# Optimization experiments

Hardware: AMD Instinct MI355X
Metric: run time of the kernel (lower is better)

## Reference

```python
import jax, jax.numpy as jnp
import numpy as np

VARIANCES = jnp.array([0.1, 0.1, 0.2, 0.2], jnp.float32)
TOTAL_LABELS = 81
MAX_TOTAL = 200        # max_total_size (also max_output_size_per_class)
SCORE_T = 0.5          # score_threshold
IOU_T = 0.5            # tf combined_non_max_suppression default iou_threshold


def setup_inputs() -> dict:
    key = jax.random.key(0)
    k1, k2, k3, k4 = jax.random.split(key, 4)
    B, N, C = 8, 1000, TOTAL_LABELS
    # valid normalized RoIs: y1,x1 in [0,0.7), h,w in [0.01,0.31)
    yx1 = jax.random.uniform(k1, (B, N, 2), jnp.float32) * 0.7
    hw = jax.random.uniform(k2, (B, N, 2), jnp.float32) * 0.3 + 0.01
    roi_bboxes = jnp.concatenate([yx1, yx1 + hw], axis=-1)  # [y1,x1,y2,x2]
    pred_deltas = jax.random.normal(k3, (B, N, C * 4), jnp.float32) * 0.5
    pred_label_probs = jax.random.uniform(k4, (B, N, C), jnp.float32)
    return {"roi_bboxes": roi_bboxes, "pred_deltas": pred_deltas,
            "pred_label_probs": pred_label_probs}


def _decode(rois, deltas):
    # rois: [..., 4] (y1,x1,y2,x2); deltas: [..., 4] (dy,dx,dh,dw)
    h = rois[..., 2] - rois[..., 0]
    w = rois[..., 3] - rois[..., 1]
    cy = rois[..., 0] + 0.5 * h
    cx = rois[..., 1] + 0.5 * w
    ncy = deltas[..., 0] * h + cy
    ncx = deltas[..., 1] * w + cx
    nh = jnp.exp(deltas[..., 2]) * h
    nw = jnp.exp(deltas[..., 3]) * w
    return jnp.stack([ncy - 0.5 * nh, ncx - 0.5 * nw,
                      ncy + 0.5 * nh, ncx + 0.5 * nw], axis=-1)


def _nms_lane(boxes, scores):
    # greedy per-class NMS over one (batch, class) lane. boxes [N,4], scores [N]
    N = boxes.shape[0]
    order = jnp.argsort(-scores)
    b = boxes[order]
    s = scores[order]
    area = (b[:, 2] - b[:, 0]) * (b[:, 3] - b[:, 1])
    idx = jnp.arange(N)

    def body(i, keep):
        bi = b[i]
        iy1 = jnp.maximum(bi[0], b[:, 0])
        ix1 = jnp.maximum(bi[1], b[:, 1])
        iy2 = jnp.minimum(bi[2], b[:, 2])
        ix2 = jnp.minimum(bi[3], b[:, 3])
        inter = jnp.maximum(iy2 - iy1, 0.0) * jnp.maximum(ix2 - ix1, 0.0)
        iou = inter / (area[i] + area - inter + 1e-8)
        suppress = keep[i] & (iou > IOU_T) & (idx > i)
        return keep & ~suppress

    keep0 = s > SCORE_T                       # score filtering before NMS
    keep = jax.lax.fori_loop(0, N, body, keep0)
    keep = keep & (jnp.cumsum(keep) <= MAX_TOTAL)  # max_output_size_per_class
    return b, jnp.where(keep, s, 0.0)          # boxes in score order, masked scores


def _forward(roi_bboxes, pred_deltas, pred_label_probs):
    B, N, _ = pred_deltas.shape
    C = TOTAL_LABELS
    deltas = pred_deltas.reshape(B, N, C, 4) * VARIANCES
    boxes = _decode(roi_bboxes[:, :, None, :], deltas)          # [B,N,C,4]
    bg = jnp.argmax(pred_label_probs, axis=-1)[..., None] == 0  # background rows
    scores = jnp.where(bg, 0.0, pred_label_probs)               # [B,N,C]

    boxes_t = boxes.transpose(0, 2, 1, 3)   # [B,C,N,4]
    scores_t = scores.transpose(0, 2, 1)    # [B,C,N]
    b_s, s_s = jax.vmap(jax.vmap(_nms_lane))(boxes_t, scores_t)

    flat_s = s_s.reshape(B, C * N)
    flat_b = b_s.reshape(B, C * N, 4)
    cls = jnp.broadcast_to(jnp.arange(C)[:, None], (C, N)).reshape(C * N)

    top_s, top_i = jax.lax.top_k(flat_s, MAX_TOTAL)             # combined top-k
    top_b = jnp.take_along_axis(flat_b, top_i[..., None], axis=1)
    top_c = cls[top_i]

    valid = top_s > 0.0
    final_b = jnp.clip(jnp.where(valid[..., None], top_b, 0.0), 0.0, 1.0)
    final_c = jnp.where(valid, top_c, 0).astype(jnp.float32)
    final_s = jnp.where(valid, top_s, 0.0)
    return final_b, final_c, final_s


def reference(roi_bboxes, pred_deltas, pred_label_probs):
    return _forward(roi_bboxes, pred_deltas, pred_label_probs)
```

## Files before the change

### kernel.cpp

```cpp
#include <hip/hip_runtime.h>

#define NROI 1000
#define NCLS 81
#define NB   8
#define NLANE (NB*NCLS)
#define MAXM 1024
#define MAXKEEP 200
#define SCORE_T 0.5f
#define NT 512
#define NW 8
#define SCAP 1024
#define TROWS 125

typedef unsigned long long u64;
typedef unsigned int u32;


__device__ __forceinline__ void decode_box(const float* __restrict__ roi,
                                           const float* __restrict__ dl,
                                           float& oy1, float& ox1,
                                           float& oy2, float& ox2) {
#pragma clang fp contract(off)
  float y1 = roi[0], x1 = roi[1], y2 = roi[2], x2 = roi[3];
  float h = y2 - y1;
  float w = x2 - x1;
  float cy = y1 + 0.5f * h;
  float cx = x1 + 0.5f * w;
  float d0 = dl[0] * 0.1f;
  float d1 = dl[1] * 0.1f;
  float d2 = dl[2] * 0.2f;
  float d3 = dl[3] * 0.2f;
  float ncy = d0 * h + cy;
  float ncx = d1 * w + cx;
  float nh = expf(d2) * h;
  float nw = expf(d3) * w;
  oy1 = ncy - 0.5f * nh;
  ox1 = ncx - 0.5f * nw;
  oy2 = ncy + 0.5f * nh;
  ox2 = ncx + 0.5f * nw;
}

__device__ __forceinline__ float area_f(float4 bx) {
#pragma clang fp contract(off)
  return (bx.z - bx.x) * (bx.w - bx.y);
}

__device__ __forceinline__ bool hit_f(float4 bi, float ia, float4 bj, float ja) {
#pragma clang fp contract(off)
  float yy1 = fmaxf(bi.x, bj.x);
  float xx1 = fmaxf(bi.y, bj.y);
  float yy2 = fminf(bi.z, bj.z);
  float xx2 = fminf(bi.w, bj.w);
  float ih = fmaxf(yy2 - yy1, 0.0f);
  float iw = fmaxf(xx2 - xx1, 0.0f);
  float inter = ih * iw;
  float den = ia + ja;
  den = den - inter;
  den = den + 1e-8f;
  return (inter + inter) > den;
}

__device__ __forceinline__ u64 pack_key(u32 sbits, int flat, int n) {
  return ((u64)sbits << 32) | ((u64)(131071 - flat) << 15) | ((u64)n << 5);
}

__global__ __launch_bounds__(512) void prep_kernel(const float* __restrict__ probs,
                                                   float* __restrict__ probs_t,
                                                   int* __restrict__ bhist) {
  __shared__ float tile[TROWS * NCLS];
  __shared__ u32 bgf[TROWS];
  int blk = blockIdx.x;
  int tid = threadIdx.x;
  if (blk == 0) {
    for (int i = tid; i < NB * 256; i += 512) bhist[i] = 0;
  }
  int row0 = blk * TROWS;
  for (int i = tid; i < TROWS * NCLS; i += 512)
    tile[i] = probs[(size_t)row0 * NCLS + i];
  __syncthreads();
  if (tid < TROWS) {
    const float* r = &tile[tid * NCLS];
    float p0 = r[0], m = -1e30f;
    for (int c2 = 1; c2 < NCLS; ++c2) m = fmaxf(m, r[c2]);
    bgf[tid] = (p0 >= m) ? 1u : 0u;
  }
  __syncthreads();
  int b = row0 / NROI;
  int nbase = row0 - b * NROI;
  for (int j = tid; j < TROWS * NCLS; j += 512) {
    int c2 = j / TROWS, r = j - c2 * TROWS;
    float v = bgf[r] ? 0.0f : tile[r * NCLS + c2];
    probs_t[((size_t)(b * NCLS + c2)) * NROI + nbase + r] = v;
  }
}

__global__ __launch_bounds__(NT) void gather_nms_kernel(
    const float* __restrict__ roi, const float* __restrict__ deltas,
    const float* __restrict__ probs_t,
    int* __restrict__ keep_count, u64* __restrict__ lane_key,
    int* __restrict__ bhist) {
  int lane = (blockIdx.x % 8) * NCLS + blockIdx.x / 8;
  int b = lane / NCLS, c = lane % NCLS;
  int tid = threadIdx.x;
  int w = tid >> 6, l = tid & 63;

  __shared__ alignas(16) char smem[26624];
  float4* sbox   = (float4*)smem;
  u64*    skeyU  = (u64*)smem;
  u64*    skeyB  = (u64*)(smem + 8192);
  u64*    skey   = (u64*)(smem + 16384);
  int*    bcnt   = (int*)(smem + 24576);
  int*    bstart = (int*)(smem + 25600);
  __shared__ u64 hmask8[NW][64];
  __shared__ u64 suppm8[NW];
  __shared__ u64 keepmask[16];
  __shared__ int scount, segbase[16];

  if (tid == 0) scount = 0;
  if (tid < 256) bcnt[tid] = 0;
  __syncthreads();

  const float* pc = probs_t + ((size_t)(b * NCLS + c)) * NROI;
  for (int base_n = 0; base_n < NROI; base_n += NT) {
    int n = base_n + tid;
    float s = (n < NROI) ? pc[n] : 0.0f;
    bool cand = s > SCORE_T;
    u64 bal = __ballot(cand);
    int wb = 0;
    if (l == 0) wb = atomicAdd(&scount, (int)__popcll(bal));
    wb = __shfl(wb, 0);
    if (cand) {
      int off = (int)__popcll(bal & ((1ull << l) - 1ull));
      u32 sb = __float_as_uint(s);
      skeyU[wb + off] = ((u64)sb << 32) | (u64)(0xFFFFFFFFu - (u32)n);
      atomicAdd(&bcnt[(sb >> 15) & 255], 1);
    }
  }
  __syncthreads();
  int M = scount;
  int nchunks = (M + 63) >> 6;

  if (w == 0) {
    int d0 = 4 * l, d1 = d0 + 1, d2 = d0 + 2, d3 = d0 + 3;
    int c0 = bcnt[255 - d0], c1 = bcnt[255 - d1];
    int c2 = bcnt[255 - d2], c3 = bcnt[255 - d3];
    int t = c0 + c1 + c2 + c3;
    int inc = t;
    for (int off = 1; off < 64; off <<= 1) {
      int v = __shfl_up(inc, off);
      if (l >= off) inc += v;
    }
    int excl = inc - t;
    int s0 = excl, s1 = excl + c0, s2 = excl + c0 + c1, s3 = excl + c0 + c1 + c2;
    bcnt[255 - d0] = s0; bstart[255 - d0] = s0;
    bcnt[255 - d1] = s1; bstart[255 - d1] = s1;
    bcnt[255 - d2] = s2; bstart[255 - d2] = s2;
    bcnt[255 - d3] = s3; bstart[255 - d3] = s3;
  }
  __syncthreads();

  for (int p = tid; p < M; p += NT) {
    u64 k = skeyU[p];
    int bkt = (int)((k >> 47) & 255);
    int pos = atomicAdd(&bcnt[bkt], 1);
    skeyB[pos] = k;
  }
  __syncthreads();

  for (int p = tid; p < M; p += NT) {
    u64 k = skeyB[p];
    int bkt = (int)((k >> 47) & 255);
    int st = bstart[bkt], en = bcnt[bkt];
    int r = st;
    for (int q = st; q < en; ++q) r += (skeyB[q] > k) ? 1 : 0;
    skey[r] = k;
  }
  if (tid < 16) {
    int rem = M - (tid << 6);
    keepmask[tid] = (rem >= 64) ? ~0ull : ((rem <= 0) ? 0ull : ((1ull << rem) - 1ull));
  }
  __syncthreads();

  if (w == 7 && nchunks > 0) {
    u64 k = skey[l];
    int nn = (int)(0xFFFFFFFFu - (u32)(k & 0xFFFFFFFFull));
    int row = b * NROI + ((l < M) ? nn : 0);
    float by1, bx1, by2, bx2;
    decode_box(roi + (size_t)row * 4, deltas + ((size_t)row * NCLS + c) * 4,
               by1, bx1, by2, bx2);
    sbox[l] = make_float4(by1, bx1, by2, bx2);
  }
  __syncthreads();

  int kc = 0;
  const u64 stridemask = 0x0101010101010101ull << w;
  const u64 low = (1ull << l) - 1ull;
  for (int ck = 0; ck < nchunks; ++ck) {
    int start = ck << 6;
    float4 bj = sbox[start + l];
    float ja = area_f(bj);

    {
      u64 part = 0;
#pragma unroll
      for (int r = 0; r < 8; ++r) {
        int i = (w << 3) + r;
        float4 bi = sbox[start + i];
        float ia = area_f(bi);
        if (hit_f(bi, ia, bj, ja)) part |= (1ull << i);
      }
      hmask8[w][l] = part;
    }

    {
      bool supp = false;
      for (int q = 0; q < ck; ++q) {
        u64 mq = keepmask[q] & stridemask;
        while (mq) {
          int i = __ffsll((unsigned long long)mq) - 1;
          mq &= mq - 1;
          float4 bi = sbox[(q << 6) + i];
          float ia = area_f(bi);
          supp |= hit_f(bi, ia, bj, ja);
        }
      }
      u64 sb = __ballot(supp);
      if (l == 0) suppm8[w] = sb;
    }

    if (w == 7 && ck + 1 < nchunks) {
      int p = ((ck + 1) << 6) + l;
      u64 k = skey[p];
      int nn = (int)(0xFFFFFFFFu - (u32)(k & 0xFFFFFFFFull));
      int row = b * NROI + ((p < M) ? nn : 0);
      float by1, bx1, by2, bx2;
      decode_box(roi + (size_t)row * 4, deltas + ((size_t)row * NCLS + c) * 4,
                 by1, bx1, by2, bx2);
      sbox[p] = make_float4(by1, bx1, by2, bx2);
    }
    __syncthreads();

    u64 rowm = hmask8[0][l] | hmask8[1][l] | hmask8[2][l] | hmask8[3][l]
             | hmask8[4][l] | hmask8[5][l] | hmask8[6][l] | hmask8[7][l];
    u64 sall = suppm8[0] | suppm8[1] | suppm8[2] | suppm8[3]
             | suppm8[4] | suppm8[5] | suppm8[6] | suppm8[7];
    int rem0 = M - start;
    u64 alive = (rem0 >= 64) ? ~0ull : ((rem0 <= 0) ? 0ull : ((1ull << rem0) - 1ull));
    u64 und = alive & ~sall;
    u64 kept = 0;
    while (und) {
      bool isu = (und >> l) & 1;
      bool su = isu && ((rowm & kept & low) != 0ull);
      bool ke = isu && ((rowm & (kept | und) & low) == 0ull);
      u64 sm = __ballot(su);
      u64 km2 = __ballot(ke);
      kept |= km2;
      und &= ~(sm | km2);
    }
    if (tid == 0) keepmask[ck] = kept;
    kc += (int)__popcll(kept);
    if (kc >= MAXKEEP) break;
    __syncthreads();
  }
  __syncthreads();

  if (tid < 16) {
    int acc = 0;
    for (int i = 0; i < tid; ++i) acc += (int)__popcll(keepmask[i]);
    segbase[tid] = acc;
  }
  __syncthreads();
  int total = segbase[15] + (int)__popcll(keepmask[15]);
  for (int s = 0; s < 2; ++s) {
    int seg = (w << 1) + s;
    u64 word = keepmask[seg];
    int p = (seg << 6) + l;
    if ((word >> l) & 1) {
      int rank = segbase[seg] + (int)__popcll(word & ((1ull << l) - 1ull));
      if (rank < MAXKEEP) {
        u64 k = skey[p];
        u32 sbits = (u32)(k >> 32);
        int n = (int)(0xFFFFFFFFu - (u32)(k & 0xFFFFFFFFull));
        lane_key[(size_t)lane * MAXKEEP + rank] = pack_key(sbits, c * NROI + p, n);
        atomicAdd(&bhist[b * 256 + (int)((sbits >> 15) & 255)], 1);
      }
    }
  }
  if (tid == 0) keep_count[lane] = min(total, MAXKEEP);
}

__global__ __launch_bounds__(512) void merge_kernel(
    const float* __restrict__ roi, const float* __restrict__ deltas,
    const int* __restrict__ keep_count, const u64* __restrict__ lane_key,
    const int* __restrict__ bhist,
    float* __restrict__ out_b, float* __restrict__ out_c, float* __restrict__ out_s) {
  int b = blockIdx.x;
  int tid = threadIdx.x;
  int w = tid >> 6, l = tid & 63;

  __shared__ int mhist[256];
  __shared__ int mhsuf[256];
  __shared__ int mhcur[256];
  __shared__ int mcnts[NCLS];
  __shared__ int mtot, mscnt;
  __shared__ u64 msurv[SCAP];

  if (tid < 256) mhist[tid] = bhist[b * 256 + tid];
  for (int i = tid; i < NCLS; i += 512) mcnts[i] = keep_count[b * NCLS + i];
  if (tid == 0) mscnt = 0;
  for (int t = tid; t < MAXKEEP; t += 512) {
    size_t ob = ((size_t)b * MAXKEEP + t) * 4;
    out_b[ob + 0] = 0.0f; out_b[ob + 1] = 0.0f;
    out_b[ob + 2] = 0.0f; out_b[ob + 3] = 0.0f;
    out_c[b * MAXKEEP + t] = 0.0f;
    out_s[b * MAXKEEP + t] = 0.0f;
  }
  __syncthreads();

  if (w == 0) {
    int g0 = 4 * l;
    int c0 = mhist[g0], c1 = mhist[g0 + 1], c2 = mhist[g0 + 2], c3 = mhist[g0 + 3];
    int t = c0 + c1 + c2 + c3;
    int acc = t;
    for (int off = 1; off < 64; off <<= 1) {
      int v = __shfl_down(acc, off);
      if (l + off < 64) acc += v;
    }
    if (l == 0) mtot = acc;
    int above = acc - t;
    int s3 = above, s2 = above + c3, s1 = above + c3 + c2, s0 = above + c3 + c2 + c1;
    mhsuf[g0 + 3] = s3; mhcur[g0 + 3] = s3;
    mhsuf[g0 + 2] = s2; mhcur[g0 + 2] = s2;
    mhsuf[g0 + 1] = s1; mhcur[g0 + 1] = s1;
    mhsuf[g0 + 0] = s0; mhcur[g0 + 0] = s0;
  }
  __syncthreads();
  int valid = (mtot < MAXKEEP) ? mtot : MAXKEEP;

  for (int s = tid; s < NCLS * MAXKEEP; s += 512) {
    int c2 = s / MAXKEEP, h = s % MAXKEEP;
    if (h < mcnts[c2]) {
      u64 k = lane_key[((size_t)(b * NCLS + c2)) * MAXKEEP + h];
      int bkt = (int)((k >> 47) & 255);
      if (mhsuf[bkt] < MAXKEEP) {
        int pos = atomicAdd(&mhcur[bkt], 1);
        if (pos < SCAP) { msurv[pos] = k; atomicAdd(&mscnt, 1); }
      }
    }
  }
  __syncthreads();
  int scnt = min(mscnt, SCAP);

  for (int p = tid; p < scnt; p += 512) {
    u64 k = msurv[p];
    int bkt = (int)((k >> 47) & 255);
    int st = mhsuf[bkt];
    int en = st + mhist[bkt];
    if (en > SCAP) en = SCAP;
    int r = st;
    for (int q = st; q < en; ++q) r += (msurv[q] > k) ? 1 : 0;
    if (r < valid) {
      int flat = 131071 - (int)((k >> 15) & 0x1FFFF);
      int c2 = flat / NROI;
      int n = (int)((k >> 5) & 0x3FF);
      int row = b * NROI + n;
      float by1, bx1, by2, bx2;
      decode_box(roi + (size_t)row * 4, deltas + ((size_t)row * NCLS + c2) * 4,
                 by1, bx1, by2, bx2);
      size_t ob = ((size_t)b * MAXKEEP + r) * 4;
      out_b[ob + 0] = fminf(fmaxf(by1, 0.0f), 1.0f);
      out_b[ob + 1] = fminf(fmaxf(bx1, 0.0f), 1.0f);
      out_b[ob + 2] = fminf(fmaxf(by2, 0.0f), 1.0f);
      out_b[ob + 3] = fminf(fmaxf(bx2, 0.0f), 1.0f);
      out_c[b * MAXKEEP + r] = (float)c2;
      out_s[b * MAXKEEP + r] = __uint_as_float((u32)(k >> 32));
    }
  }
}

extern "C" void kernel_launch(void* const* d_in, const int* in_sizes, int n_in,
                              void* d_out, int out_size, void* d_ws, size_t ws_size,
                              hipStream_t stream) {
  const float* roi    = (const float*)d_in[0];
  const float* deltas = (const float*)d_in[1];
  const float* probs  = (const float*)d_in[2];

  char* ws = (char*)d_ws;
  int*   bhist      = (int*)(ws);
  int*   keep_count = (int*)(ws + 8192);
  u64*   lane_key   = (u64*)(ws + 12288);
  float* probs_t    = (float*)(ws + 1052672);

  float* out_b = (float*)d_out;
  float* out_c = out_b + NB * MAXKEEP * 4;
  float* out_s = out_c + NB * MAXKEEP;

  prep_kernel<<<64, 512, 0, stream>>>(probs, probs_t, bhist);
  gather_nms_kernel<<<NLANE, NT, 0, stream>>>(roi, deltas, probs_t,
                                              keep_count, lane_key, bhist);
  merge_kernel<<<NB, 512, 0, stream>>>(roi, deltas, keep_count, lane_key, bhist,
                                       out_b, out_c, out_s);
}
```

Baseline: 70.97 us.

## Replace transposed probs buffer with per-row background flags and strided reads

Drops the prep kernel that transposed the full probability tensor into a class-major scratch buffer and replaces it with a small kernel that only computes one background flag per row (one wavefront per row). The NMS kernel now reads scores directly from the original row-major layout with a stride of 81 floats and checks the flag. This removes a full write and re-read of the transposed tensor, but each lane's score load becomes strided and uncoalesced, so the cache lines are shared across the 81 class blocks of a batch. The workspace layout is shifted to fit the flag array.

```diff
diff --git a/kernel.cpp b/kernel.cpp
--- a/kernel.cpp
+++ b/kernel.cpp
@@ -10,7 +10,6 @@
 #define NT 512
 #define NW 8
 #define SCAP 1024
-#define TROWS 125
 
 typedef unsigned long long u64;
 typedef unsigned int u32;
@@ -64,39 +63,25 @@
   return ((u64)sbits << 32) | ((u64)(131071 - flat) << 15) | ((u64)n << 5);
 }
 
-__global__ __launch_bounds__(512) void prep_kernel(const float* __restrict__ probs,
-                                                   float* __restrict__ probs_t,
-                                                   int* __restrict__ bhist) {
-  __shared__ float tile[TROWS * NCLS];
-  __shared__ u32 bgf[TROWS];
-  int blk = blockIdx.x;
-  int tid = threadIdx.x;
-  if (blk == 0) {
-    for (int i = tid; i < NB * 256; i += 512) bhist[i] = 0;
-  }
-  int row0 = blk * TROWS;
-  for (int i = tid; i < TROWS * NCLS; i += 512)
-    tile[i] = probs[(size_t)row0 * NCLS + i];
-  __syncthreads();
-  if (tid < TROWS) {
-    const float* r = &tile[tid * NCLS];
-    float p0 = r[0], m = -1e30f;
-    for (int c2 = 1; c2 < NCLS; ++c2) m = fmaxf(m, r[c2]);
-    bgf[tid] = (p0 >= m) ? 1u : 0u;
-  }
-  __syncthreads();
-  int b = row0 / NROI;
-  int nbase = row0 - b * NROI;
-  for (int j = tid; j < TROWS * NCLS; j += 512) {
-    int c2 = j / TROWS, r = j - c2 * TROWS;
-    float v = bgf[r] ? 0.0f : tile[r * NCLS + c2];
-    probs_t[((size_t)(b * NCLS + c2)) * NROI + nbase + r] = v;
-  }
+__global__ __launch_bounds__(256) void bg_kernel(const float* __restrict__ probs,
+                                                 int* __restrict__ bg,
+                                                 int* __restrict__ bhist) {
+  if (blockIdx.x < 8) {
+    bhist[blockIdx.x * 256 + threadIdx.x] = 0;
+  }
+  int row = blockIdx.x * 4 + (threadIdx.x >> 6);
+  int lane = threadIdx.x & 63;
+  if (row >= NB * NROI) return;
+  const float* p = probs + (size_t)row * NCLS;
+  float m = -1e30f;
+  for (int idx = 1 + lane; idx < NCLS; idx += 64) m = fmaxf(m, p[idx]);
+  for (int off = 32; off; off >>= 1) m = fmaxf(m, __shfl_xor(m, off));
+  if (lane == 0) bg[row] = (p[0] >= m) ? 1 : 0;
 }
 
 __global__ __launch_bounds__(NT) void gather_nms_kernel(
     const float* __restrict__ roi, const float* __restrict__ deltas,
-    const float* __restrict__ probs_t,
+    const float* __restrict__ probs, const int* __restrict__ bg,
     int* __restrict__ keep_count, u64* __restrict__ lane_key,
     int* __restrict__ bhist) {
   int lane = (blockIdx.x % 8) * NCLS + blockIdx.x / 8;
@@ -120,11 +105,15 @@
   if (tid < 256) bcnt[tid] = 0;
   __syncthreads();
 
-  const float* pc = probs_t + ((size_t)(b * NCLS + c)) * NROI;
   for (int base_n = 0; base_n < NROI; base_n += NT) {
     int n = base_n + tid;
-    float s = (n < NROI) ? pc[n] : 0.0f;
-    bool cand = s > SCORE_T;
+    bool cand = false;
+    float s = 0.0f;
+    if (n < NROI) {
+      int row = b * NROI + n;
+      s = probs[(size_t)row * NCLS + c];
+      cand = (s > SCORE_T) && (bg[row] == 0);
+    }
     u64 bal = __ballot(cand);
     int wb = 0;
     if (l == 0) wb = atomicAdd(&scount, (int)__popcll(bal));
@@ -386,17 +375,17 @@
   const float* probs  = (const float*)d_in[2];
 
   char* ws = (char*)d_ws;
-  int*   bhist      = (int*)(ws);
-  int*   keep_count = (int*)(ws + 8192);
-  u64*   lane_key   = (u64*)(ws + 12288);
-  float* probs_t    = (float*)(ws + 1052672);
+  int* bg         = (int*)(ws);
+  int* bhist      = (int*)(ws + 32768);
+  int* keep_count = (int*)(ws + 40960);
+  u64* lane_key   = (u64*)(ws + 45056);
 
   float* out_b = (float*)d_out;
   float* out_c = out_b + NB * MAXKEEP * 4;
   float* out_s = out_c + NB * MAXKEEP;
 
-  prep_kernel<<<64, 512, 0, stream>>>(probs, probs_t, bhist);
-  gather_nms_kernel<<<NLANE, NT, 0, stream>>>(roi, deltas, probs_t,
+  bg_kernel<<<(NB * NROI + 3) / 4, 256, 0, stream>>>(probs, bg, bhist);
+  gather_nms_kernel<<<NLANE, NT, 0, stream>>>(roi, deltas, probs, bg,
                                               keep_count, lane_key, bhist);
   merge_kernel<<<NB, 512, 0, stream>>>(roi, deltas, keep_count, lane_key, bhist,
                                        out_b, out_c, out_s);
```

Measured after the change: 72.50 us. 2.2% more time.
